# Kernel optimization log

Measured on AMD Instinct MI355X. Metric: run time of the kernel, lower is better.

## Reference

```python
import jax, jax.numpy as jnp
import numpy as np

N, B, M, D, K = 131072, 1024, 128, 256, 32
T1 = 0.1
GAMMA = 0.99
BN_EPS = 1e-5
LRELU_SLOPE = 0.01


def setup_inputs() -> dict:
    key = jax.random.key(0)
    ks = jax.random.split(key, 8)
    z = jax.random.normal(ks[0], (N, D), dtype=jnp.float32)
    g = jax.random.normal(ks[1], (B, D), dtype=jnp.float32)
    batch = (jnp.arange(N, dtype=jnp.int32) // M)  # B graphs, M nodes each
    W1 = jax.random.normal(ks[2], (D, D), dtype=jnp.float32) / np.sqrt(D)
    b1 = jnp.zeros((D,), jnp.float32)
    bn_gamma = jnp.ones((D,), jnp.float32)
    bn_beta = jnp.zeros((D,), jnp.float32)
    W2 = jax.random.normal(ks[3], (D, K), dtype=jnp.float32) / np.sqrt(D)
    b2 = jnp.zeros((K,), jnp.float32)
    U = jax.random.uniform(ks[4], (K, D), dtype=jnp.float32, minval=-1.5, maxval=1.5)
    return {"z": z, "g": g, "batch": batch, "W1": W1, "b1": b1,
            "bn_gamma": bn_gamma, "bn_beta": bn_beta, "W2": W2, "b2": b2, "U": U}


def _to_dense_batch(x, batch, num_graphs, max_nodes):
    # PyG to_dense_batch: scatter nodes into [B, M, ...] padded tensor + mask
    n = x.shape[0]
    counts = jax.ops.segment_sum(jnp.ones((n,), jnp.int32), batch, num_segments=num_graphs)
    offsets = jnp.concatenate([jnp.zeros((1,), jnp.int32), jnp.cumsum(counts)[:-1]])
    pos = jnp.arange(n, dtype=jnp.int32) - offsets[batch]  # index within graph
    dense = jnp.zeros((num_graphs, max_nodes) + x.shape[1:], x.dtype).at[batch, pos].set(x)
    mask = jnp.zeros((num_graphs, max_nodes), bool).at[batch, pos].set(True)
    return dense, mask


def reference(z, g, batch, W1, b1, bn_gamma, bn_beta, W2, b2, U):
    # node_classifier: Linear -> BatchNorm1d (train-mode batch stats) -> LeakyReLU -> Linear
    h1 = z @ W1 + b1
    mu = h1.mean(0)
    var = h1.var(0)  # biased, as BN normalization
    h1 = (h1 - mu) / jnp.sqrt(var + BN_EPS) * bn_gamma + bn_beta
    h1 = jnp.where(h1 > 0, h1, LRELU_SLOPE * h1)
    logits = h1 @ W2 + b2  # [N, K]
    s = jax.nn.softmax(logits / T1, axis=-1)

    z_dense, _ = _to_dense_batch(z, batch, B, M)        # [B, M, D]
    s_dense, _ = _to_dense_batch(s, batch, B, M)        # [B, M, K]

    # std-based sub-cluster filter (torch.std is unbiased, ddof=1, over cluster dim)
    std = jnp.std(s_dense, axis=-1, ddof=1, keepdims=True)
    sub_filter = s_dense > (std + 1.0 / K)
    s_dense = s_dense * sub_filter.astype(s_dense.dtype)

    p_hat = s_dense.sum(axis=1)                          # [B, K]
    p_hat = p_hat / (p_hat + 1e-12)
    p_hat = p_hat[:, :, None] * jnp.eye(K, dtype=p_hat.dtype)  # diag_embed -> [B, K, K]

    # L1-normalized soft-cluster pooling
    w = jnp.swapaxes(s_dense, 1, 2)                      # [B, K, M]
    w = w / jnp.maximum(jnp.abs(w).sum(-1, keepdims=True), 1e-12)
    h_dense = jnp.einsum('bkm,bmd->bkd', w, z_dense)     # [B, K, D]
    sub_mask = jnp.abs(h_dense).sum(-1) > 0.0            # [B, K]

    # EMA centroid update (note: original uses .view(K, B), a reshape, not transpose)
    h_perm = jnp.transpose(h_dense, (1, 0, 2))           # [K, B, D]
    mask_r = sub_mask.reshape(K, B)
    sizes = mask_r.astype(h_perm.dtype).sum(-1, keepdims=True)  # [K, 1]
    centroids = h_perm.sum(axis=1) / (sizes + 1e-10)
    centroids = jax.lax.stop_gradient(centroids)
    U_new = GAMMA * U + (1.0 - GAMMA) * centroids        # [K, D]

    # h = h_dense[sub_mask] has dynamic shape; return flat h with masked rows zeroed
    h_flat = h_dense.reshape(B * K, D) * sub_mask.reshape(-1, 1).astype(h_dense.dtype)
    hn = h_flat / jnp.maximum(jnp.linalg.norm(h_flat, axis=-1, keepdims=True), 1e-12)
    Un = U / jnp.maximum(jnp.linalg.norm(U, axis=-1, keepdims=True), 1e-12)
    p = hn @ Un.T                                        # [B*K, K] pairwise cos sim

    return (s, h_flat, h_dense, p, p_hat, z_dense, g, sub_mask, U_new)
```

## Files before the change

kernel.cpp:

```cpp
#include <hip/hip_runtime.h>
#include <math.h>

#define NN 131072
#define BBG 1024
#define MMN 128
#define DDF 256
#define KKC 32

#define OFF_S      0
#define OFF_HFLAT  4194304
#define OFF_HDENSE 12582912
#define OFF_P      20971520
#define OFF_PHAT   22020096
#define OFF_ZD     23068672
#define OFF_G      56623104
#define OFF_MASK   56885248
#define OFF_UNEW   56918016

#define WS_PSUM  0
#define WS_PSQ   524288
#define WS_TMP   1048576
#define WS_SCALE 1052672
#define WS_SHIFT 1052928
#define WS_UN    1053184
#define WS_SF    1061376
#define WS_C     5255680
#define WS_PART  5288448

typedef __attribute__((ext_vector_type(8))) short short8;
typedef __attribute__((ext_vector_type(4))) float f32x4;

__device__ __forceinline__ unsigned short f2bf(float x) {
  unsigned u = __float_as_uint(x);
  u += 0x7fffu + ((u >> 16) & 1u);
  return (unsigned short)(u >> 16);
}
__device__ __forceinline__ float bf2f(unsigned short h) {
  return __uint_as_float(((unsigned)h) << 16);
}

__global__ __launch_bounds__(256) void k0_prep(const float* __restrict__ W1,
    const float* __restrict__ U, unsigned short* __restrict__ preh,
    unsigned short* __restrict__ prel, float* __restrict__ Un)
{
  if (blockIdx.x < 32) {
    int tid = blockIdx.x * 256 + threadIdx.x;
    int n = tid & 255, kq = tid >> 8;
    short8 hv, lv;
    #pragma unroll
    for (int j = 0; j < 8; ++j) {
      float v = W1[(kq * 8 + j) * DDF + n];
      unsigned short hb = f2bf(v);
      hv[j] = (short)hb;
      lv[j] = (short)f2bf(v - bf2f(hb));
    }
    int base = (kq >> 2) * 8192 + (kq & 3) * 2048 + n * 8;
    *(short8*)(preh + base) = hv;
    *(short8*)(prel + base) = lv;
  } else {
    int k = (blockIdx.x - 32) * 4 + (threadIdx.x >> 6);
    int l = threadIdx.x & 63;
    float4 u = *(const float4*)(U + k*256 + l*4);
    float ss = u.x*u.x + u.y*u.y + u.z*u.z + u.w*u.w;
    #pragma unroll
    for (int off = 32; off >= 1; off >>= 1) ss += __shfl_xor(ss, off);
    float inv = 1.0f / fmaxf(sqrtf(ss), 1e-12f);
    *(float4*)(Un + k*256 + l*4) = make_float4(u.x*inv, u.y*inv, u.z*inv, u.w*inv);
  }
}

__global__ __launch_bounds__(512) void k1_gemm1(
    const float* __restrict__ z, const unsigned short* __restrict__ preh,
    const unsigned short* __restrict__ prel, const float* __restrict__ b1,
    float* __restrict__ h1, float* __restrict__ psum, float* __restrict__ psq)
{
  __shared__ __attribute__((aligned(16))) unsigned short Ah[8][64 * 40];
  __shared__ __attribute__((aligned(16))) unsigned short Al[8][64 * 40];

  const int t = threadIdx.x;
  const int l = t & 63;
  const int w = t >> 6;
  const int wr = w >> 2;
  const int wc = w & 3;
  const int lg = l >> 4;
  const int l16 = l & 15;
  const int n0 = blockIdx.x * 128;

  unsigned short* myAh = Ah[w];
  unsigned short* myAl = Al[w];

  f32x4 acc[4][4];
  #pragma unroll
  for (int i = 0; i < 4; ++i)
    #pragma unroll
    for (int j = 0; j < 4; ++j) acc[i][j] = (f32x4)0.0f;

  const int row0 = l >> 3;
  const int c4 = l & 7;
  const float* zw = z + (size_t)(n0 + wr * 64) * DDF;
  const unsigned short* bhbase = preh + lg * 2048 + wc * 512 + l16 * 8;
  const unsigned short* blbase = prel + lg * 2048 + wc * 512 + l16 * 8;

#define CVTSTORE(ZR) do { \
    _Pragma("unroll") \
    for (int i = 0; i < 8; ++i) { \
      float4 v = ZR[i]; \
      unsigned short h0 = f2bf(v.x), h1v = f2bf(v.y), h2 = f2bf(v.z), h3 = f2bf(v.w); \
      uint2 hp = make_uint2((unsigned)h0 | ((unsigned)h1v << 16), \
                            (unsigned)h2 | ((unsigned)h3 << 16)); \
      uint2 lp = make_uint2((unsigned)f2bf(v.x - bf2f(h0)) | ((unsigned)f2bf(v.y - bf2f(h1v)) << 16), \
                            (unsigned)f2bf(v.z - bf2f(h2)) | ((unsigned)f2bf(v.w - bf2f(h3)) << 16)); \
      *(uint2*)(&myAh[(row0 + 8*i) * 40 + c4 * 4]) = hp; \
      *(uint2*)(&myAl[(row0 + 8*i) * 40 + c4 * 4]) = lp; \
    } } while (0)

#define ZLOAD(ZR, KS) do { \
    _Pragma("unroll") \
    for (int i = 0; i < 8; ++i) \
      ZR[i] = *(const float4*)(zw + (size_t)(row0 + 8*i) * DDF + (KS) * 32 + c4 * 4); \
  } while (0)

  float4 zr[8];
  ZLOAD(zr, 0);
  CVTSTORE(zr);
  ZLOAD(zr, 1);

  #pragma unroll
  for (int ks = 0; ks < 8; ++ks) {
    short8 bfh[4], bfl[4];
    #pragma unroll
    for (int nf = 0; nf < 4; ++nf) {
      bfh[nf] = *(const short8*)(bhbase + ks * 8192 + nf * 128);
      bfl[nf] = *(const short8*)(blbase + ks * 8192 + nf * 128);
    }
    __builtin_amdgcn_s_setprio(1);
    #pragma unroll
    for (int mf = 0; mf < 4; ++mf) {
      const int ar = mf * 16 + l16;
      short8 afh = *(const short8*)(&myAh[ar * 40 + lg * 8]);
      short8 afl = *(const short8*)(&myAl[ar * 40 + lg * 8]);
      #pragma unroll
      for (int nf = 0; nf < 4; ++nf)
        acc[mf][nf] = __builtin_amdgcn_mfma_f32_16x16x32_bf16(afh, bfh[nf], acc[mf][nf], 0, 0, 0);
      #pragma unroll
      for (int nf = 0; nf < 4; ++nf)
        acc[mf][nf] = __builtin_amdgcn_mfma_f32_16x16x32_bf16(afl, bfh[nf], acc[mf][nf], 0, 0, 0);
      #pragma unroll
      for (int nf = 0; nf < 4; ++nf)
        acc[mf][nf] = __builtin_amdgcn_mfma_f32_16x16x32_bf16(afh, bfl[nf], acc[mf][nf], 0, 0, 0);
    }
    __builtin_amdgcn_s_setprio(0);
    if (ks < 7) {
      CVTSTORE(zr);
      if (ks < 6) ZLOAD(zr, ks + 2);
    }
  }
#undef CVTSTORE
#undef ZLOAD

  float s1[4] = {0, 0, 0, 0}, s2[4] = {0, 0, 0, 0};
  #pragma unroll
  for (int nf = 0; nf < 4; ++nf) {
    int c = wc * 64 + nf * 16 + l16;
    float bb = b1[c];
    #pragma unroll
    for (int mf = 0; mf < 4; ++mf) {
      int rbase = n0 + wr * 64 + mf * 16 + lg * 4;
      #pragma unroll
      for (int j = 0; j < 4; ++j) {
        float v = acc[mf][nf][j] + bb;
        s1[nf] += v; s2[nf] += v * v;
        h1[(size_t)(rbase + j) * DDF + c] = v;
      }
    }
  }
  #pragma unroll
  for (int nf = 0; nf < 4; ++nf) {
    s1[nf] += __shfl_xor(s1[nf], 16); s1[nf] += __shfl_xor(s1[nf], 32);
    s2[nf] += __shfl_xor(s2[nf], 16); s2[nf] += __shfl_xor(s2[nf], 32);
  }
  __syncthreads();
  float* red1 = (float*)Ah;
  float* red2 = (float*)Al;
  if (l < 16) {
    #pragma unroll
    for (int nf = 0; nf < 4; ++nf) {
      red1[wr * 256 + wc * 64 + nf * 16 + l] = s1[nf];
      red2[wr * 256 + wc * 64 + nf * 16 + l] = s2[nf];
    }
  }
  __syncthreads();
  if (t < 256) {
    psum[blockIdx.x * 256 + t] = red1[t] + red1[256 + t];
    psq [blockIdx.x * 256 + t] = red2[t] + red2[256 + t];
  }
}

__global__ __launch_bounds__(256) void k2a(const float* __restrict__ psum,
                                           const float* __restrict__ psq,
                                           float* __restrict__ tmp)
{
  int g = blockIdx.x & 7;
  const float* src = (blockIdx.x < 8) ? psum : psq;
  float acc = 0.f;
  #pragma unroll 8
  for (int r = 0; r < 128; ++r) acc += src[(g * 128 + r) * 256 + threadIdx.x];
  tmp[blockIdx.x * 256 + threadIdx.x] = acc;
}

__global__ __launch_bounds__(256) void k2b(const float* __restrict__ tmp,
    const float* __restrict__ gam, const float* __restrict__ bet,
    float* __restrict__ scale, float* __restrict__ shift)
{
  int d = threadIdx.x;
  float s1 = 0.f, s2 = 0.f;
  #pragma unroll
  for (int g = 0; g < 8; ++g) { s1 += tmp[g*256+d]; s2 += tmp[(8+g)*256+d]; }
  float mu  = s1 * (1.0f / (float)NN);
  float var = s2 * (1.0f / (float)NN) - mu*mu;
  float inv = 1.0f / sqrtf(var + 1e-5f);
  float sc = gam[d] * inv;
  scale[d] = sc;
  shift[d] = bet[d] - mu*sc;
}

__global__ __launch_bounds__(256) void k3_gemm2(
    const float* __restrict__ h1, const float* __restrict__ W2,
    const float* __restrict__ b2, const float* __restrict__ scale,
    const float* __restrict__ shift, float* __restrict__ s_out,
    float* __restrict__ sf_out)
{
  __shared__ float ylds[4][64*32];
  const int t = threadIdx.x;
  const int w = t >> 6, l = t & 63;
  const int b = blockIdx.x * 2 + (w >> 1);
  const int half = w & 1;
  const int rowbase = b * MMN + half * 64;
  float* my = ylds[w];
  const int lx7 = l & 7;
  const int rsub = l >> 3;

  float acc[32];
  #pragma unroll
  for (int k = 0; k < 32; ++k) acc[k] = 0.f;

  for (int ch = 0; ch < 8; ++ch) {
    const float4 sc = *(const float4*)(scale + ch*32 + lx7*4);
    const float4 sh = *(const float4*)(shift + ch*32 + lx7*4);
    #pragma unroll
    for (int i = 0; i < 8; ++i) {
      int row = rsub + i*8;
      float4 v = *(const float4*)(h1 + (size_t)(rowbase + row)*DDF + ch*32 + lx7*4);
      float y0 = fmaf(v.x, sc.x, sh.x); y0 = y0 > 0.f ? y0 : 0.01f*y0;
      float y1 = fmaf(v.y, sc.y, sh.y); y1 = y1 > 0.f ? y1 : 0.01f*y1;
      float y2 = fmaf(v.z, sc.z, sh.z); y2 = y2 > 0.f ? y2 : 0.01f*y2;
      float y3 = fmaf(v.w, sc.w, sh.w); y3 = y3 > 0.f ? y3 : 0.01f*y3;
      *(float4*)(&my[row*32 + (lx7 ^ rsub)*4]) = make_float4(y0,y1,y2,y3);
    }
    #pragma unroll
    for (int d4 = 0; d4 < 8; ++d4) {
      float4 ya = *(const float4*)(&my[l*32 + (d4 ^ lx7)*4]);
      #pragma unroll
      for (int dd = 0; dd < 4; ++dd) {
        const float* w2r = W2 + (ch*32 + d4*4 + dd)*KKC;
        float a = (dd==0?ya.x: dd==1?ya.y: dd==2?ya.z: ya.w);
        #pragma unroll
        for (int k = 0; k < 32; ++k) acc[k] = fmaf(a, w2r[k], acc[k]);
      }
    }
  }
  #pragma unroll
  for (int k = 0; k < 32; ++k) acc[k] = (acc[k] + b2[k]) * 10.0f;
  float thr;
  {
    float m = acc[0];
    #pragma unroll
    for (int k = 1; k < 32; ++k) m = fmaxf(m, acc[k]);
    float sum = 0.f;
    #pragma unroll
    for (int k = 0; k < 32; ++k) { float e = expf(acc[k]-m); acc[k] = e; sum += e; }
    float inv = 1.0f/sum;
    float ssum = 0.f;
    #pragma unroll
    for (int k = 0; k < 32; ++k) { acc[k] *= inv; ssum += acc[k]; }
    float mean = ssum * (1.0f/32.0f);
    float var = 0.f;
    #pragma unroll
    for (int k = 0; k < 32; ++k) { float d = acc[k]-mean; var += d*d; }
    thr = sqrtf(var * (1.0f/31.0f)) + 0.03125f;
  }
  #pragma unroll
  for (int q = 0; q < 8; ++q)
    *(float4*)(&my[l*32 + (q ^ lx7)*4]) =
        make_float4(acc[q*4],acc[q*4+1],acc[q*4+2],acc[q*4+3]);
  #pragma unroll
  for (int i = 0; i < 8; ++i) {
    int fid = l + i*64;
    int row = fid >> 3, q = fid & 7;
    *(float4*)(s_out + (size_t)rowbase*KKC + fid*4) =
        *(const float4*)(&my[row*32 + (q ^ (row & 7))*4]);
  }
  #pragma unroll
  for (int k = 0; k < 32; ++k) acc[k] = acc[k] > thr ? acc[k] : 0.f;
  #pragma unroll
  for (int q = 0; q < 8; ++q)
    *(float4*)(&my[l*32 + (q ^ lx7)*4]) =
        make_float4(acc[q*4],acc[q*4+1],acc[q*4+2],acc[q*4+3]);
  #pragma unroll
  for (int i = 0; i < 8; ++i) {
    int fid = l + i*64;
    int row = fid >> 3, q = fid & 7;
    *(float4*)(sf_out + (size_t)rowbase*KKC + fid*4) =
        *(const float4*)(&my[row*32 + (q ^ (row & 7))*4]);
  }
}

__global__ __launch_bounds__(256) void k4_pool(
    const float* __restrict__ sf, const float* __restrict__ z,
    float* __restrict__ c_out, float* __restrict__ hdense,
    float* __restrict__ hflat, float* __restrict__ mask_out,
    float* __restrict__ zd, float* __restrict__ phat,
    const float* __restrict__ g, float* __restrict__ gout)
{
  __shared__ __align__(16) float sflds[128*32];
  __shared__ __align__(16) float zlds[16*256];
  __shared__ float redp[8*32];
  __shared__ float cred[32];

  const int t = threadIdx.x;
  const int w = t >> 6, l = t & 63;
  const int b = blockIdx.x;

  gout[b*256 + t] = g[b*256 + t];

  #pragma unroll
  for (int i = 0; i < 4; ++i) {
    int fid = t + i*256;
    *(float4*)(&sflds[fid*4]) = *(const float4*)(sf + (size_t)b*4096 + fid*4);
  }
  __syncthreads();
  {
    int k = t & 31, mg = t >> 5;
    float p = 0.f;
    #pragma unroll
    for (int m = 0; m < 16; ++m) p += sflds[(mg*16+m)*32 + k];
    redp[mg*32 + k] = p;
  }
  __syncthreads();
  if (t < 32) {
    float c = 0.f;
    #pragma unroll
    for (int g2 = 0; g2 < 8; ++g2) c += redp[g2*32 + t];
    cred[t] = c;
    c_out[b*32 + t] = c;
  }
  __syncthreads();
  {
    float cc = cred[t >> 3];
    float pv = cc / (cc + 1e-12f);
    int k1r = t >> 3;
    float4 ph;
    ph.x = (((t*4+0) & 31) == k1r) ? pv : 0.f;
    ph.y = (((t*4+1) & 31) == k1r) ? pv : 0.f;
    ph.z = (((t*4+2) & 31) == k1r) ? pv : 0.f;
    ph.w = (((t*4+3) & 31) == k1r) ? pv : 0.f;
    *(float4*)(phat + (size_t)b*1024 + t*4) = ph;
  }

  float acc[8][4];
  #pragma unroll
  for (int kk = 0; kk < 8; ++kk)
    #pragma unroll
    for (int j = 0; j < 4; ++j) acc[kk][j] = 0.f;

  for (int ch = 0; ch < 8; ++ch) {
    #pragma unroll
    for (int i = 0; i < 4; ++i) {
      int fid = t + i*256;
      float4 v = *(const float4*)(z + (size_t)(b*128 + ch*16)*256 + fid*4);
      *(float4*)(&zlds[fid*4]) = v;
      *(float4*)(zd + (size_t)(b*128 + ch*16)*256 + fid*4) = v;
    }
    __syncthreads();
    #pragma unroll
    for (int mm = 0; mm < 16; ++mm) {
      float4 zv = *(const float4*)(&zlds[mm*256 + l*4]);
      float4 sa = *(const float4*)(&sflds[(ch*16+mm)*32 + w*8]);
      float4 sb = *(const float4*)(&sflds[(ch*16+mm)*32 + w*8 + 4]);
      float sv[8] = {sa.x,sa.y,sa.z,sa.w,sb.x,sb.y,sb.z,sb.w};
      #pragma unroll
      for (int kk = 0; kk < 8; ++kk) {
        acc[kk][0] = fmaf(sv[kk], zv.x, acc[kk][0]);
        acc[kk][1] = fmaf(sv[kk], zv.y, acc[kk][1]);
        acc[kk][2] = fmaf(sv[kk], zv.z, acc[kk][2]);
        acc[kk][3] = fmaf(sv[kk], zv.w, acc[kk][3]);
      }
    }
    __syncthreads();
  }
  float asum[8], mkarr[8];
  #pragma unroll
  for (int kk = 0; kk < 8; ++kk) {
    float wnv = 1.0f / fmaxf(cred[w*8+kk], 1e-12f);
    acc[kk][0]*=wnv; acc[kk][1]*=wnv; acc[kk][2]*=wnv; acc[kk][3]*=wnv;
    asum[kk] = fabsf(acc[kk][0])+fabsf(acc[kk][1])+fabsf(acc[kk][2])+fabsf(acc[kk][3]);
  }
  #pragma unroll
  for (int kk = 0; kk < 8; ++kk) {
    float a = asum[kk];
    #pragma unroll
    for (int off = 1; off < 64; off <<= 1) a += __shfl_xor(a, off);
    asum[kk] = a;
  }
  #pragma unroll
  for (int kk = 0; kk < 8; ++kk) {
    int krow = b*32 + w*8 + kk;
    float mk = asum[kk] > 0.f ? 1.0f : 0.0f;
    mkarr[kk] = mk;
    float h0=acc[kk][0], h1v=acc[kk][1], h2=acc[kk][2], h3=acc[kk][3];
    *(float4*)(hdense + (size_t)krow*256 + l*4) = make_float4(h0,h1v,h2,h3);
    *(float4*)(hflat  + (size_t)krow*256 + l*4) =
        make_float4(h0*mk,h1v*mk,h2*mk,h3*mk);
  }
  if (l == 0) {
    #pragma unroll
    for (int kk = 0; kk < 8; ++kk) mask_out[b*32 + w*8 + kk] = mkarr[kk];
  }
}

__global__ __launch_bounds__(256) void k4b_p(
    const float* __restrict__ hflat, const float* __restrict__ Un,
    float* __restrict__ p_out)
{
  __shared__ float hl[32*260];
  __shared__ float ul[32*256];
  const int t = threadIdx.x;
  const int b = blockIdx.x;

  #pragma unroll
  for (int i = 0; i < 8; ++i) {
    int fid = t + i*256;
    int row = fid >> 6, c4 = fid & 63;
    *(float4*)(&hl[row*260 + c4*4]) =
        *(const float4*)(hflat + (size_t)b*8192 + fid*4);
    *(float4*)(&ul[fid*4]) = *(const float4*)(Un + fid*4);
  }
  __syncthreads();
  {
    const int k = t & 31, k2 = (t >> 5) * 4;
    float p0=0.f, p1=0.f, p2=0.f, p3=0.f, qq=0.f;
    #pragma unroll 8
    for (int d4 = 0; d4 < 64; ++d4) {
      float4 hv = *(const float4*)(&hl[k*260 + d4*4]);
      qq = fmaf(hv.x,hv.x,fmaf(hv.y,hv.y,fmaf(hv.z,hv.z,fmaf(hv.w,hv.w,qq))));
      float4 u0 = *(const float4*)(&ul[(k2+0)*256 + d4*4]);
      float4 u1 = *(const float4*)(&ul[(k2+1)*256 + d4*4]);
      float4 u2 = *(const float4*)(&ul[(k2+2)*256 + d4*4]);
      float4 u3 = *(const float4*)(&ul[(k2+3)*256 + d4*4]);
      p0 = fmaf(hv.x,u0.x,fmaf(hv.y,u0.y,fmaf(hv.z,u0.z,fmaf(hv.w,u0.w,p0))));
      p1 = fmaf(hv.x,u1.x,fmaf(hv.y,u1.y,fmaf(hv.z,u1.z,fmaf(hv.w,u1.w,p1))));
      p2 = fmaf(hv.x,u2.x,fmaf(hv.y,u2.y,fmaf(hv.z,u2.z,fmaf(hv.w,u2.w,p2))));
      p3 = fmaf(hv.x,u3.x,fmaf(hv.y,u3.y,fmaf(hv.z,u3.z,fmaf(hv.w,u3.w,p3))));
    }
    float inv = 1.0f / fmaxf(sqrtf(qq), 1e-12f);
    *(float4*)(p_out + (size_t)(b*32 + k)*32 + k2) =
        make_float4(p0*inv, p1*inv, p2*inv, p3*inv);
  }
}

__global__ __launch_bounds__(256) void k5a(const float* __restrict__ hdense,
                                           float* __restrict__ part)
{
  int k = blockIdx.x & 31, seg = blockIdx.x >> 5;
  int t = threadIdx.x;
  float s = 0.f;
  #pragma unroll 4
  for (int i = 0; i < 128; ++i) {
    int b = seg*128 + i;
    s += hdense[(size_t)(b*32 + k)*256 + t];
  }
  part[blockIdx.x*256 + t] = s;
}

__global__ __launch_bounds__(256) void k5b(const float* __restrict__ part,
    const float* __restrict__ maskf, const float* __restrict__ U,
    float* __restrict__ Unew)
{
  __shared__ float r4[4];
  int k = blockIdx.x, t = threadIdx.x;
  float4 mv = *(const float4*)(maskf + k*1024 + t*4);
  float m4 = mv.x + mv.y + mv.z + mv.w;
  #pragma unroll
  for (int off = 1; off < 64; off <<= 1) m4 += __shfl_xor(m4, off);
  if ((t & 63) == 0) r4[t >> 6] = m4;
  __syncthreads();
  float sizes = r4[0] + r4[1] + r4[2] + r4[3];
  float csum = 0.f;
  #pragma unroll
  for (int g = 0; g < 8; ++g) csum += part[(g*32 + k)*256 + t];
  float cent = csum / (sizes + 1e-10f);
  Unew[k*256 + t] = 0.99f * U[k*256 + t] + 0.01f * cent;
}

extern "C" void kernel_launch(void* const* d_in, const int* in_sizes, int n_in,
                              void* d_out, int out_size, void* d_ws, size_t ws_size,
                              hipStream_t stream)
{
  const float* z   = (const float*)d_in[0];
  const float* g   = (const float*)d_in[1];
  const float* W1  = (const float*)d_in[3];
  const float* b1  = (const float*)d_in[4];
  const float* gam = (const float*)d_in[5];
  const float* bet = (const float*)d_in[6];
  const float* W2  = (const float*)d_in[7];
  const float* b2  = (const float*)d_in[8];
  const float* U   = (const float*)d_in[9];
  float* out = (float*)d_out;
  float* ws  = (float*)d_ws;

  float* h1 = out + OFF_ZD;
  unsigned short* preh = (unsigned short*)(out + OFF_S);
  unsigned short* prel = preh + 65536;

  k0_prep<<<40, 256, 0, stream>>>(W1, U, preh, prel, ws+WS_UN);
  k1_gemm1<<<1024, 512, 0, stream>>>(z, preh, prel, b1, h1, ws+WS_PSUM, ws+WS_PSQ);
  k2a<<<16, 256, 0, stream>>>(ws+WS_PSUM, ws+WS_PSQ, ws+WS_TMP);
  k2b<<<1, 256, 0, stream>>>(ws+WS_TMP, gam, bet, ws+WS_SCALE, ws+WS_SHIFT);
  k3_gemm2<<<512, 256, 0, stream>>>(h1, W2, b2, ws+WS_SCALE, ws+WS_SHIFT,
                                    out+OFF_S, ws+WS_SF);
  k4_pool<<<1024, 256, 0, stream>>>(ws+WS_SF, z, ws+WS_C,
                                    out+OFF_HDENSE, out+OFF_HFLAT,
                                    out+OFF_MASK, out+OFF_ZD,
                                    out+OFF_PHAT, g, out+OFF_G);
  k4b_p<<<1024, 256, 0, stream>>>(out+OFF_HFLAT, ws+WS_UN, out+OFF_P);
  k5a<<<256, 256, 0, stream>>>(out+OFF_HDENSE, ws+WS_PART);
  k5b<<<32, 256, 0, stream>>>(ws+WS_PART, out+OFF_MASK, U, out+OFF_UNEW);
}
```

Before: 306.4 us.

## Restructure GEMM1 to 64-row blocks with whole-tile LDS staging of z

```diff
diff --git a/kernel.cpp b/kernel.cpp
--- a/kernel.cpp
+++ b/kernel.cpp
@@ -69,25 +69,35 @@
   }
 }
 
-__global__ __launch_bounds__(512) void k1_gemm1(
+__global__ __launch_bounds__(256) void k1_gemm1(
     const float* __restrict__ z, const unsigned short* __restrict__ preh,
     const unsigned short* __restrict__ prel, const float* __restrict__ b1,
     float* __restrict__ h1, float* __restrict__ psum, float* __restrict__ psq)
 {
-  __shared__ __attribute__((aligned(16))) unsigned short Ah[8][64 * 40];
-  __shared__ __attribute__((aligned(16))) unsigned short Al[8][64 * 40];
+  __shared__ __attribute__((aligned(16))) unsigned short Ah[64 * 260];
+  __shared__ __attribute__((aligned(16))) unsigned short Al[64 * 260];
 
   const int t = threadIdx.x;
   const int l = t & 63;
   const int w = t >> 6;
-  const int wr = w >> 2;
-  const int wc = w & 3;
   const int lg = l >> 4;
   const int l16 = l & 15;
-  const int n0 = blockIdx.x * 128;
-
-  unsigned short* myAh = Ah[w];
-  unsigned short* myAl = Al[w];
+  const int n0 = blockIdx.x * 64;
+
+  #pragma unroll
+  for (int i = 0; i < 16; ++i) {
+    int fid = i * 256 + t;
+    int row = fid >> 6, c = fid & 63;
+    float4 v = *(const float4*)(z + (size_t)(n0 + row) * DDF + c * 4);
+    unsigned short h0 = f2bf(v.x), h1v = f2bf(v.y), h2 = f2bf(v.z), h3 = f2bf(v.w);
+    uint2 hp = make_uint2((unsigned)h0 | ((unsigned)h1v << 16),
+                          (unsigned)h2 | ((unsigned)h3 << 16));
+    uint2 lp = make_uint2((unsigned)f2bf(v.x - bf2f(h0)) | ((unsigned)f2bf(v.y - bf2f(h1v)) << 16),
+                          (unsigned)f2bf(v.z - bf2f(h2)) | ((unsigned)f2bf(v.w - bf2f(h3)) << 16));
+    *(uint2*)(&Ah[row * 260 + c * 4]) = hp;
+    *(uint2*)(&Al[row * 260 + c * 4]) = lp;
+  }
+  __syncthreads();
 
   f32x4 acc[4][4];
   #pragma unroll
@@ -95,35 +105,8 @@
     #pragma unroll
     for (int j = 0; j < 4; ++j) acc[i][j] = (f32x4)0.0f;
 
-  const int row0 = l >> 3;
-  const int c4 = l & 7;
-  const float* zw = z + (size_t)(n0 + wr * 64) * DDF;
-  const unsigned short* bhbase = preh + lg * 2048 + wc * 512 + l16 * 8;
-  const unsigned short* blbase = prel + lg * 2048 + wc * 512 + l16 * 8;
-
-#define CVTSTORE(ZR) do { \
-    _Pragma("unroll") \
-    for (int i = 0; i < 8; ++i) { \
-      float4 v = ZR[i]; \
-      unsigned short h0 = f2bf(v.x), h1v = f2bf(v.y), h2 = f2bf(v.z), h3 = f2bf(v.w); \
-      uint2 hp = make_uint2((unsigned)h0 | ((unsigned)h1v << 16), \
-                            (unsigned)h2 | ((unsigned)h3 << 16)); \
-      uint2 lp = make_uint2((unsigned)f2bf(v.x - bf2f(h0)) | ((unsigned)f2bf(v.y - bf2f(h1v)) << 16), \
-                            (unsigned)f2bf(v.z - bf2f(h2)) | ((unsigned)f2bf(v.w - bf2f(h3)) << 16)); \
-      *(uint2*)(&myAh[(row0 + 8*i) * 40 + c4 * 4]) = hp; \
-      *(uint2*)(&myAl[(row0 + 8*i) * 40 + c4 * 4]) = lp; \
-    } } while (0)
-
-#define ZLOAD(ZR, KS) do { \
-    _Pragma("unroll") \
-    for (int i = 0; i < 8; ++i) \
-      ZR[i] = *(const float4*)(zw + (size_t)(row0 + 8*i) * DDF + (KS) * 32 + c4 * 4); \
-  } while (0)
-
-  float4 zr[8];
-  ZLOAD(zr, 0);
-  CVTSTORE(zr);
-  ZLOAD(zr, 1);
+  const unsigned short* bhbase = preh + lg * 2048 + w * 512 + l16 * 8;
+  const unsigned short* blbase = prel + lg * 2048 + w * 512 + l16 * 8;
 
   #pragma unroll
   for (int ks = 0; ks < 8; ++ks) {
@@ -136,9 +119,9 @@
     __builtin_amdgcn_s_setprio(1);
     #pragma unroll
     for (int mf = 0; mf < 4; ++mf) {
-      const int ar = mf * 16 + l16;
-      short8 afh = *(const short8*)(&myAh[ar * 40 + lg * 8]);
-      short8 afl = *(const short8*)(&myAl[ar * 40 + lg * 8]);
+      const int ro = (mf * 16 + l16) * 260 + ks * 32 + lg * 8;
+      short8 afh = *(const short8*)(&Ah[ro]);
+      short8 afl = *(const short8*)(&Al[ro]);
       #pragma unroll
       for (int nf = 0; nf < 4; ++nf)
         acc[mf][nf] = __builtin_amdgcn_mfma_f32_16x16x32_bf16(afh, bfh[nf], acc[mf][nf], 0, 0, 0);
@@ -150,22 +133,16 @@
         acc[mf][nf] = __builtin_amdgcn_mfma_f32_16x16x32_bf16(afh, bfl[nf], acc[mf][nf], 0, 0, 0);
     }
     __builtin_amdgcn_s_setprio(0);
-    if (ks < 7) {
-      CVTSTORE(zr);
-      if (ks < 6) ZLOAD(zr, ks + 2);
-    }
-  }
-#undef CVTSTORE
-#undef ZLOAD
+  }
 
   float s1[4] = {0, 0, 0, 0}, s2[4] = {0, 0, 0, 0};
   #pragma unroll
   for (int nf = 0; nf < 4; ++nf) {
-    int c = wc * 64 + nf * 16 + l16;
+    int c = w * 64 + nf * 16 + l16;
     float bb = b1[c];
     #pragma unroll
     for (int mf = 0; mf < 4; ++mf) {
-      int rbase = n0 + wr * 64 + mf * 16 + lg * 4;
+      int rbase = n0 + mf * 16 + lg * 4;
       #pragma unroll
       for (int j = 0; j < 4; ++j) {
         float v = acc[mf][nf][j] + bb;
@@ -179,20 +156,12 @@
     s1[nf] += __shfl_xor(s1[nf], 16); s1[nf] += __shfl_xor(s1[nf], 32);
     s2[nf] += __shfl_xor(s2[nf], 16); s2[nf] += __shfl_xor(s2[nf], 32);
   }
-  __syncthreads();
-  float* red1 = (float*)Ah;
-  float* red2 = (float*)Al;
   if (l < 16) {
     #pragma unroll
     for (int nf = 0; nf < 4; ++nf) {
-      red1[wr * 256 + wc * 64 + nf * 16 + l] = s1[nf];
-      red2[wr * 256 + wc * 64 + nf * 16 + l] = s2[nf];
-    }
-  }
-  __syncthreads();
-  if (t < 256) {
-    psum[blockIdx.x * 256 + t] = red1[t] + red1[256 + t];
-    psq [blockIdx.x * 256 + t] = red2[t] + red2[256 + t];
+      psum[blockIdx.x * 256 + w * 64 + nf * 16 + l] = s1[nf];
+      psq [blockIdx.x * 256 + w * 64 + nf * 16 + l] = s2[nf];
+    }
   }
 }
 
@@ -204,7 +173,7 @@
   const float* src = (blockIdx.x < 8) ? psum : psq;
   float acc = 0.f;
   #pragma unroll 8
-  for (int r = 0; r < 128; ++r) acc += src[(g * 128 + r) * 256 + threadIdx.x];
+  for (int r = 0; r < 256; ++r) acc += src[(g * 256 + r) * 256 + threadIdx.x];
   tmp[blockIdx.x * 256 + threadIdx.x] = acc;
 }
 
@@ -523,7 +492,7 @@
   unsigned short* prel = preh + 65536;
 
   k0_prep<<<40, 256, 0, stream>>>(W1, U, preh, prel, ws+WS_UN);
-  k1_gemm1<<<1024, 512, 0, stream>>>(z, preh, prel, b1, h1, ws+WS_PSUM, ws+WS_PSQ);
+  k1_gemm1<<<2048, 256, 0, stream>>>(z, preh, prel, b1, h1, ws+WS_PSUM, ws+WS_PSQ);
   k2a<<<16, 256, 0, stream>>>(ws+WS_PSUM, ws+WS_PSQ, ws+WS_TMP);
   k2b<<<1, 256, 0, stream>>>(ws+WS_TMP, gam, bet, ws+WS_SCALE, ws+WS_SHIFT);
   k3_gemm2<<<512, 256, 0, stream>>>(h1, W2, b2, ws+WS_SCALE, ws+WS_SHIFT,
```

After: 296.1 us. 1.03x faster.
